# Kernel optimization log

Hardware: AMD Instinct MI355X
Metric: run time of the kernel (lower is better)

Reference implementation:

```python
import jax, jax.numpy as jnp
import numpy as np

B, L, D, H, FF, V, NL = 1024, 200, 128, 4, 512, 100001, 2
DK = D // H
EPS = 1e-5


def layer_norm(x, w, b):
    mu = jnp.mean(x, axis=-1, keepdims=True)
    var = jnp.mean(jnp.square(x - mu), axis=-1, keepdims=True)
    return (x - mu) * jax.lax.rsqrt(var + EPS) * w + b


def setup_inputs() -> dict:
    key = jax.random.key(0)
    ks = jax.random.split(key, 32)
    s = 0.02
    d = {}
    d["batch_seqs"] = jax.random.randint(ks[0], (B, L), 0, V, dtype=jnp.int32)
    d["token_emb"] = jax.random.normal(ks[1], (V, D), jnp.float32) * s
    d["pos_emb"] = jax.random.normal(ks[2], (L, D), jnp.float32) * s
    # per-layer stacked params, leading axis = layer
    d["Wq"] = jax.random.normal(ks[3], (NL, D, D), jnp.float32) * s
    d["bq"] = jnp.zeros((NL, D), jnp.float32)
    d["Wk"] = jax.random.normal(ks[4], (NL, D, D), jnp.float32) * s
    d["bk"] = jnp.zeros((NL, D), jnp.float32)
    d["Wv"] = jax.random.normal(ks[5], (NL, D, D), jnp.float32) * s
    d["bv"] = jnp.zeros((NL, D), jnp.float32)
    d["Wo"] = jax.random.normal(ks[6], (NL, D, D), jnp.float32) * s
    d["bo"] = jnp.zeros((NL, D), jnp.float32)
    d["ln1_w"] = jnp.ones((NL, D), jnp.float32)
    d["ln1_b"] = jnp.zeros((NL, D), jnp.float32)
    d["ln2_w"] = jnp.ones((NL, D), jnp.float32)
    d["ln2_b"] = jnp.zeros((NL, D), jnp.float32)
    d["W1"] = jax.random.normal(ks[7], (NL, D, FF), jnp.float32) * s
    d["b1"] = jnp.zeros((NL, FF), jnp.float32)
    d["W2"] = jax.random.normal(ks[8], (NL, FF, D), jnp.float32) * s
    d["b2"] = jnp.zeros((NL, D), jnp.float32)
    d["fc_W"] = jax.random.normal(ks[9], (L * D, D), jnp.float32) * s
    d["fc_b"] = jnp.zeros((D,), jnp.float32)
    return d


def reference(batch_seqs, token_emb, pos_emb, Wq, bq, Wk, bk, Wv, bv, Wo, bo,
              ln1_w, ln1_b, ln2_w, ln2_b, W1, b1, W2, b2, fc_W, fc_b):
    # key-padding mask: [B,1,1,L] (broadcasts over heads and queries)
    mask = (batch_seqs > 0)[:, None, None, :]
    x = token_emb[batch_seqs] + pos_emb[None, :, :]  # [B,L,D]
    scale = 1.0 / jnp.sqrt(jnp.float32(DK))
    for i in range(NL):
        h = layer_norm(x, ln1_w[i], ln1_b[i])
        q = (h @ Wq[i] + bq[i]).reshape(B, L, H, DK)
        k = (h @ Wk[i] + bk[i]).reshape(B, L, H, DK)
        v = (h @ Wv[i] + bv[i]).reshape(B, L, H, DK)
        scores = jnp.einsum('bqhd,bkhd->bhqk', q, k) * scale
        scores = jnp.where(mask, scores, -1e9)
        p = jax.nn.softmax(scores, axis=-1)
        attn = jnp.einsum('bhqk,bkhd->bqhd', p, v).reshape(B, L, D)
        x = x + (attn @ Wo[i] + bo[i])
        h = layer_norm(x, ln2_w[i], ln2_b[i])
        ffn = jax.nn.gelu(h @ W1[i] + b1[i], approximate=False) @ W2[i] + b2[i]
        x = x + ffn
    # FlattenLayers: flatten [B, L*D] -> Linear -> [B, D]
    out = x.reshape(B, L * D) @ fc_W + fc_b
    return out
```

## Files before the change

### kernel.cpp

```cpp
#include <hip/hip_runtime.h>
#include <math.h>

typedef unsigned short u16;
typedef unsigned int u32;
typedef __attribute__((ext_vector_type(8))) short bf16x8;
typedef __attribute__((ext_vector_type(4))) float f32x4;

#define Bx 1024
#define Lx 200
#define Dx 128
#define FFx 512
#define Mx (Bx*Lx)
#define PVP 232
#define TSP 40

__device__ __forceinline__ u16 f2bf(float f) {
  u32 u = __float_as_uint(f);
  u32 r = (u + 0x7fffu + ((u >> 16) & 1u)) >> 16;
  return (u16)r;
}

__device__ __forceinline__ float gelu_f(float v) {
  float z = v * fmaf(v * v, 0.0713548163f, 1.5957691216f);
  float e = __expf(-z);
  return v * __builtin_amdgcn_rcpf(1.0f + e);
}

union BFCV { u32 u[4]; bf16x8 h; };

__global__ void k_cvt(const float* __restrict__ src, u16* __restrict__ dst,
                      int N, int k_steps) {
  int id = blockIdx.x * 256 + threadIdx.x;
  int lane = id & 63;
  int rest = id >> 6;
  int kst = rest % k_steps;
  int ntile = rest / k_steps;
  int n = ntile * 16 + (lane & 15);
  int kb = kst * 32 + ((lane >> 4) << 3);
  const float* sp = src + (size_t)kb * N + n;
  u32 w[4];
  #pragma unroll
  for (int j = 0; j < 4; ++j) {
    u32 lo = f2bf(sp[(size_t)(2 * j) * N]);
    u32 hi = f2bf(sp[(size_t)(2 * j + 1) * N]);
    w[j] = lo | (hi << 16);
  }
  ((uint4*)dst)[id] = make_uint4(w[0], w[1], w[2], w[3]);
}

__global__ void k_embed(const int* __restrict__ seq, const float* __restrict__ tok,
                        const float* __restrict__ pos, float* __restrict__ x) {
  const int i = blockIdx.x * 256 + threadIdx.x;
  const int row = i >> 5, c = i & 31;
  const int t = seq[row];
  const int l = row % Lx;
  const float4 a = ((const float4*)tok)[(size_t)t * 32 + c];
  const float4 p = ((const float4*)pos)[l * 32 + c];
  ((float4*)x)[i] = make_float4(a.x + p.x, a.y + p.y, a.z + p.z, a.w + p.w);
}

__device__ __forceinline__ void reg_ln(const float* __restrict__ xr,
                                       const float* __restrict__ ln_w,
                                       const float* __restrict__ ln_b,
                                       int quad, bf16x8 af[4]) {
  float v[32];
  float s = 0.f, sq = 0.f;
  #pragma unroll
  for (int kst = 0; kst < 4; ++kst) {
    float4 a = *(const float4*)(xr + kst * 32);
    float4 b = *(const float4*)(xr + kst * 32 + 4);
    v[kst * 8 + 0] = a.x; v[kst * 8 + 1] = a.y; v[kst * 8 + 2] = a.z; v[kst * 8 + 3] = a.w;
    v[kst * 8 + 4] = b.x; v[kst * 8 + 5] = b.y; v[kst * 8 + 6] = b.z; v[kst * 8 + 7] = b.w;
  }
  #pragma unroll
  for (int i = 0; i < 32; ++i) { s += v[i]; sq = fmaf(v[i], v[i], sq); }
  s  += __shfl_xor(s, 16);  s  += __shfl_xor(s, 32);
  sq += __shfl_xor(sq, 16); sq += __shfl_xor(sq, 32);
  float mu = s * 0.0078125f;
  float rr = rsqrtf(fmaf(-mu, mu, sq * 0.0078125f) + 1e-5f);
  #pragma unroll
  for (int kst = 0; kst < 4; ++kst) {
    const float* lwp = ln_w + kst * 32 + quad * 8;
    const float* lbp = ln_b + kst * 32 + quad * 8;
    float4 lw0 = *(const float4*)(lwp);
    float4 lw1 = *(const float4*)(lwp + 4);
    float4 lb0 = *(const float4*)(lbp);
    float4 lb1 = *(const float4*)(lbp + 4);
    float hw[8] = {lw0.x, lw0.y, lw0.z, lw0.w, lw1.x, lw1.y, lw1.z, lw1.w};
    float hb[8] = {lb0.x, lb0.y, lb0.z, lb0.w, lb1.x, lb1.y, lb1.z, lb1.w};
    BFCV cv;
    #pragma unroll
    for (int j = 0; j < 4; ++j) {
      float h0 = fmaf((v[kst * 8 + 2 * j]     - mu) * rr, hw[2 * j],     hb[2 * j]);
      float h1 = fmaf((v[kst * 8 + 2 * j + 1] - mu) * rr, hw[2 * j + 1], hb[2 * j + 1]);
      cv.u[j] = (u32)f2bf(h0) | ((u32)f2bf(h1) << 16);
    }
    af[kst] = cv.h;
  }
}

__global__ __launch_bounds__(256, 4)
void k_qkv(const float* __restrict__ x, const float* __restrict__ ln_w,
           const float* __restrict__ ln_b, const u16* __restrict__ Wqkvs,
           const float* __restrict__ bq, const float* __restrict__ bk,
           const float* __restrict__ bv,
           u16* __restrict__ qo, u16* __restrict__ ko, u16* __restrict__ vo) {
  const int tid = threadIdx.x;
  const int row0 = blockIdx.x * 64;
  const int lane = tid & 63, wv = tid >> 6;
  const int l15 = lane & 15, quad = lane >> 4;
  const int m0 = wv * 16;

  bf16x8 af[4];
  reg_ln(x + (size_t)(row0 + m0 + l15) * Dx + quad * 8, ln_w, ln_b, quad, af);

  int bl[4], ll[4];
  #pragma unroll
  for (int r = 0; r < 4; ++r) {
    int gr = row0 + m0 + quad * 4 + r;
    bl[r] = gr / 200;
    ll[r] = gr - bl[r] * 200;
  }

  const float scale = 0.17677669529663687f;
  #pragma unroll
  for (int nt = 0; nt < 24; ++nt) {
    f32x4 acc = (f32x4){0.f, 0.f, 0.f, 0.f};
    const u16* wb = Wqkvs + ((size_t)(nt * 4) * 64 + lane) * 8;
    #pragma unroll
    for (int kst = 0; kst < 4; ++kst) {
      bf16x8 bfr = *(const bf16x8*)(wb + kst * 64 * 8);
      acc = __builtin_amdgcn_mfma_f32_16x16x32_bf16(af[kst], bfr, acc, 0, 0, 0);
    }
    const int col = (nt & 7) * 16 + l15;
    const int head = col >> 5, dk = col & 31;
    if (nt < 8) {
      float bb = bq[col];
      #pragma unroll
      for (int r = 0; r < 4; ++r)
        qo[((size_t)(bl[r] * 4 + head) * 200 + ll[r]) * 32 + dk] = f2bf((acc[r] + bb) * scale);
    } else if (nt < 16) {
      float bb = bk[col];
      #pragma unroll
      for (int r = 0; r < 4; ++r)
        ko[((size_t)(bl[r] * 4 + head) * 200 + ll[r]) * 32 + dk] = f2bf(acc[r] + bb);
    } else {
      float bb = bv[col];
      #pragma unroll
      for (int r = 0; r < 4; ++r)
        vo[((size_t)(bl[r] * 4 + head) * 200 + ll[r]) * 32 + dk] = f2bf(acc[r] + bb);
    }
  }
}

__global__ __launch_bounds__(256, 3)
void k_attn2(const u16* __restrict__ q, const u16* __restrict__ k,
             const u16* __restrict__ v, const int* __restrict__ seq,
             u16* __restrict__ attn) {
  __shared__ float smask[224];
  __shared__ __align__(16) u16 vt[32 * PVP];
  __shared__ __align__(16) u16 Pb[4][16 * PVP];
  const int tid = threadIdx.x;
  const int bl = blockIdx.x >> 2, head = blockIdx.x & 3;
  const int bh = blockIdx.x;
  const int lane = tid & 63, wv = tid >> 6;
  const int l15 = lane & 15, quad = lane >> 4;

  if (tid < 224)
    smask[tid] = (tid < 200 && seq[bl * 200 + tid] > 0) ? 0.f : -1e9f;
  #pragma unroll 1
  for (int e = tid; e < 800; e += 256) {
    int l = e >> 2, g = (e & 3) * 8;
    uint4 pv = *(const uint4*)(v + ((size_t)bh * 200 + l) * 32 + g);
    const u16* pw = (const u16*)&pv;
    #pragma unroll
    for (int j = 0; j < 8; ++j) vt[(g + j) * PVP + l] = pw[j];
  }
  #pragma unroll 1
  for (int e = tid; e < 1024; e += 256) {
    int rr = e >> 5, cc = 200 + (e & 31);
    vt[rr * PVP + cc] = 0;
  }
  __syncthreads();

  float msk[14];
  #pragma unroll
  for (int nt = 0; nt < 14; ++nt) msk[nt] = smask[nt * 16 + l15];

  const u16* qbase = q + (size_t)bh * 200 * 32;
  const u16* kbase = k + (size_t)bh * 200 * 32;
  u16* Pw = Pb[wv];

  #pragma unroll 1
  for (int mt = wv; mt < 13; mt += 4) {
    bf16x8 qf = *(const bf16x8*)(qbase + (mt * 16 + l15) * 32 + quad * 8);
    f32x4 s[14];
    #pragma unroll
    for (int nt = 0; nt < 14; ++nt) {
      bf16x8 kf = *(const bf16x8*)(kbase + (nt * 16 + l15) * 32 + quad * 8);
      s[nt] = __builtin_amdgcn_mfma_f32_16x16x32_bf16(qf, kf, (f32x4){0.f, 0.f, 0.f, 0.f}, 0, 0, 0);
    }
    float rmax[4] = {-1e30f, -1e30f, -1e30f, -1e30f};
    #pragma unroll
    for (int nt = 0; nt < 14; ++nt) {
      #pragma unroll
      for (int r = 0; r < 4; ++r) {
        s[nt][r] += msk[nt];
        rmax[r] = fmaxf(rmax[r], s[nt][r]);
      }
    }
    #pragma unroll
    for (int m = 1; m < 16; m <<= 1) {
      #pragma unroll
      for (int r = 0; r < 4; ++r) rmax[r] = fmaxf(rmax[r], __shfl_xor(rmax[r], m));
    }
    float rsum[4] = {0.f, 0.f, 0.f, 0.f};
    #pragma unroll
    for (int nt = 0; nt < 14; ++nt) {
      #pragma unroll
      for (int r = 0; r < 4; ++r) {
        float p = __expf(s[nt][r] - rmax[r]);
        s[nt][r] = p;
        rsum[r] += p;
      }
    }
    #pragma unroll
    for (int m = 1; m < 16; m <<= 1) {
      #pragma unroll
      for (int r = 0; r < 4; ++r) rsum[r] += __shfl_xor(rsum[r], m);
    }
    float inv[4];
    #pragma unroll
    for (int r = 0; r < 4; ++r) inv[r] = 1.0f / rsum[r];
    #pragma unroll
    for (int nt = 0; nt < 14; ++nt) {
      #pragma unroll
      for (int r = 0; r < 4; ++r)
        Pw[(quad * 4 + r) * PVP + nt * 16 + l15] = f2bf(s[nt][r]);
    }
    __asm__ __volatile__("s_waitcnt lgkmcnt(0)" ::: "memory");
    f32x4 o0 = (f32x4){0.f, 0.f, 0.f, 0.f}, o1 = (f32x4){0.f, 0.f, 0.f, 0.f};
    #pragma unroll
    for (int kst = 0; kst < 7; ++kst) {
      bf16x8 pf  = *(const bf16x8*)&Pw[l15 * PVP + kst * 32 + quad * 8];
      bf16x8 vf0 = *(const bf16x8*)&vt[l15 * PVP + kst * 32 + quad * 8];
      bf16x8 vf1 = *(const bf16x8*)&vt[(16 + l15) * PVP + kst * 32 + quad * 8];
      o0 = __builtin_amdgcn_mfma_f32_16x16x32_bf16(pf, vf0, o0, 0, 0, 0);
      o1 = __builtin_amdgcn_mfma_f32_16x16x32_bf16(pf, vf1, o1, 0, 0, 0);
    }
    #pragma unroll
    for (int r = 0; r < 4; ++r) {
      int row = mt * 16 + quad * 4 + r;
      if (row < 200) {
        u16* op = attn + ((size_t)bl * 200 + row) * 128 + head * 32;
        op[l15]      = f2bf(o0[r] * inv[r]);
        op[16 + l15] = f2bf(o1[r] * inv[r]);
      }
    }
  }
}

__global__ __launch_bounds__(256, 4)
void k_oproj(const u16* __restrict__ a, const u16* __restrict__ Wos,
             const float* __restrict__ bo, float* __restrict__ x) {
  const int tid = threadIdx.x;
  const int lane = tid & 63, wv = tid >> 6;
  const int l15 = lane & 15, quad = lane >> 4;
  const size_t m0 = (size_t)blockIdx.x * 64 + wv * 16;
  f32x4 acc[8];
  #pragma unroll
  for (int i = 0; i < 8; ++i) acc[i] = (f32x4){0.f, 0.f, 0.f, 0.f};
  #pragma unroll
  for (int kst = 0; kst < 4; ++kst) {
    bf16x8 af = *(const bf16x8*)(a + (m0 + l15) * Dx + kst * 32 + quad * 8);
    const u16* wb = Wos + (kst * 64 + lane) * 8;
    #pragma unroll
    for (int nt = 0; nt < 8; ++nt) {
      bf16x8 bf = *(const bf16x8*)(wb + nt * (4 * 64 * 8));
      acc[nt] = __builtin_amdgcn_mfma_f32_16x16x32_bf16(af, bf, acc[nt], 0, 0, 0);
    }
  }
  #pragma unroll
  for (int nt = 0; nt < 8; ++nt) {
    int col = nt * 16 + l15;
    float bb = bo[col];
    #pragma unroll
    for (int r = 0; r < 4; ++r) {
      size_t idx = (m0 + quad * 4 + r) * Dx + col;
      x[idx] += acc[nt][r] + bb;
    }
  }
}

__global__ __launch_bounds__(512, 4)
void k_ffn(float* __restrict__ x, const float* __restrict__ ln_w,
           const float* __restrict__ ln_b,
           const u16* __restrict__ W1s, const float* __restrict__ b1,
           const u16* __restrict__ W2s, const float* __restrict__ b2) {
  __shared__ __align__(16) u16 smem[5120 + 8192 + 8192];
  u16* ts  = smem;
  u16* w1b = smem + 5120;
  u16* w2b = smem + 13312;
  const int tid = threadIdx.x;
  const size_t row0 = (size_t)blockIdx.x * 128;
  const int lane = tid & 63, wv = tid >> 6;
  const int l15 = lane & 15, quad = lane >> 4;
  const int m0 = wv * 16;
  const int snt = wv, soff = lane;

  bf16x8 af[4];
  reg_ln(x + (row0 + m0 + l15) * (size_t)Dx + quad * 8, ln_w, ln_b, quad, af);

  ((uint4*)w1b)[tid] = ((const uint4*)(W1s + (size_t)(snt * 4) * 512))[soff];
  ((uint4*)w2b)[tid] = ((const uint4*)(W2s + (size_t)(snt * 16) * 512))[soff];
  __syncthreads();

  f32x4 acc2[8];
  #pragma unroll
  for (int i = 0; i < 8; ++i) acc2[i] = (f32x4){0.f, 0.f, 0.f, 0.f};

  #pragma unroll 1
  for (int ch = 0; ch < 4; ++ch) {
    f32x4 acc1[8];
    #pragma unroll
    for (int i = 0; i < 8; ++i) acc1[i] = (f32x4){0.f, 0.f, 0.f, 0.f};
    #pragma unroll
    for (int kst = 0; kst < 4; ++kst) {
      uint4 stg;
      if (kst < 3)
        stg = ((const uint4*)(W1s + (size_t)((ch * 8 + snt) * 4 + kst + 1) * 512))[soff];
      const u16* wb = w1b + (kst & 1) * 4096;
      #pragma unroll
      for (int nt = 0; nt < 8; ++nt) {
        bf16x8 bfr = *(const bf16x8*)&wb[nt * 512 + lane * 8];
        acc1[nt] = __builtin_amdgcn_mfma_f32_16x16x32_bf16(af[kst], bfr, acc1[nt], 0, 0, 0);
      }
      if (kst < 3)
        ((uint4*)(w1b + ((kst + 1) & 1) * 4096))[tid] = stg;
      __syncthreads();
    }
    #pragma unroll
    for (int p = 0; p < 4; ++p) {
      uint4 stg2, stg1;
      const bool s2  = (p < 3);
      const bool s1n = (p == 3) && (ch < 3);
      if (s2)
        stg2 = ((const uint4*)(W2s + (size_t)(snt * 16 + ch * 4 + p + 1) * 512))[soff];
      if (s1n) {
        stg1 = ((const uint4*)(W1s + (size_t)((ch + 1) * 8 + snt) * 4 * 512))[soff];
        stg2 = ((const uint4*)(W2s + (size_t)(snt * 16 + (ch + 1) * 4) * 512))[soff];
      }
      #pragma unroll
      for (int q2 = 0; q2 < 2; ++q2) {
        const int ntg = 2 * p + q2;
        float bb = b1[ch * 128 + ntg * 16 + l15];
        #pragma unroll
        for (int r = 0; r < 4; ++r)
          ts[(m0 + quad * 4 + r) * TSP + q2 * 16 + l15] =
              f2bf(gelu_f(acc1[ntg][r] + bb));
      }
      __asm__ __volatile__("s_waitcnt lgkmcnt(0)" ::: "memory");
      bf16x8 tf = *(const bf16x8*)&ts[(m0 + l15) * TSP + quad * 8];
      const u16* wb = w2b + (p & 1) * 4096;
      #pragma unroll
      for (int nt = 0; nt < 8; ++nt) {
        bf16x8 bfr = *(const bf16x8*)&wb[nt * 512 + lane * 8];
        acc2[nt] = __builtin_amdgcn_mfma_f32_16x16x32_bf16(tf, bfr, acc2[nt], 0, 0, 0);
      }
      if (s2)
        ((uint4*)(w2b + ((p + 1) & 1) * 4096))[tid] = stg2;
      if (s1n) {
        ((uint4*)w1b)[tid] = stg1;
        ((uint4*)w2b)[tid] = stg2;
      }
      __syncthreads();
    }
  }
  #pragma unroll
  for (int nt = 0; nt < 8; ++nt) {
    int col = nt * 16 + l15;
    float bb = b2[col];
    #pragma unroll
    for (int r = 0; r < 4; ++r) {
      size_t idx = (row0 + m0 + quad * 4 + r) * Dx + col;
      x[idx] += acc2[nt][r] + bb;
    }
  }
}

__global__ __launch_bounds__(256, 4)
void k_fc(const float* __restrict__ x, const u16* __restrict__ fcWs,
          float* __restrict__ part) {
  const int tid = threadIdx.x;
  const int lane = tid & 63, wv = tid >> 6;
  const int l15 = lane & 15, quad = lane >> 4;
  const int m0 = blockIdx.x * 64 + wv * 16;
  const int ky = blockIdx.y;
  f32x4 acc[8];
  #pragma unroll
  for (int i = 0; i < 8; ++i) acc[i] = (f32x4){0.f, 0.f, 0.f, 0.f};
  const float* xp = x + (size_t)(m0 + l15) * 25600 + quad * 8;
  #pragma unroll 1
  for (int kst = ky * 25; kst < ky * 25 + 25; ++kst) {
    float4 xa = *(const float4*)(xp + kst * 32);
    float4 xb2 = *(const float4*)(xp + kst * 32 + 4);
    bf16x8 af;
    af[0] = (short)f2bf(xa.x);  af[1] = (short)f2bf(xa.y);
    af[2] = (short)f2bf(xa.z);  af[3] = (short)f2bf(xa.w);
    af[4] = (short)f2bf(xb2.x); af[5] = (short)f2bf(xb2.y);
    af[6] = (short)f2bf(xb2.z); af[7] = (short)f2bf(xb2.w);
    const u16* wb = fcWs + ((size_t)kst * 64 + lane) * 8;
    #pragma unroll
    for (int nt = 0; nt < 8; ++nt) {
      bf16x8 bf = *(const bf16x8*)(wb + (size_t)nt * (800 * 64 * 8));
      acc[nt] = __builtin_amdgcn_mfma_f32_16x16x32_bf16(af, bf, acc[nt], 0, 0, 0);
    }
  }
  float* pp = part + (size_t)ky * (Bx * Dx);
  #pragma unroll
  for (int nt = 0; nt < 8; ++nt) {
    #pragma unroll
    for (int r = 0; r < 4; ++r) {
      pp[(size_t)(m0 + quad * 4 + r) * Dx + nt * 16 + l15] = acc[nt][r];
    }
  }
}

__global__ void k_fcred(const float* __restrict__ part, const float* __restrict__ fcb,
                        float* __restrict__ out) {
  int i = blockIdx.x * 256 + threadIdx.x;
  float s = fcb[i & 127];
  #pragma unroll
  for (int k = 0; k < 32; ++k) s += part[(size_t)k * (Bx * Dx) + i];
  out[i] = s;
}

extern "C" void kernel_launch(void* const* d_in, const int* in_sizes, int n_in,
                              void* d_out, int out_size, void* d_ws, size_t ws_size,
                              hipStream_t stream) {
  const int*   seq  = (const int*)d_in[0];
  const float* tok  = (const float*)d_in[1];
  const float* pos  = (const float*)d_in[2];
  const float* Wq   = (const float*)d_in[3];
  const float* bq   = (const float*)d_in[4];
  const float* Wk   = (const float*)d_in[5];
  const float* bk   = (const float*)d_in[6];
  const float* Wv   = (const float*)d_in[7];
  const float* bv   = (const float*)d_in[8];
  const float* Wo   = (const float*)d_in[9];
  const float* bo   = (const float*)d_in[10];
  const float* ln1w = (const float*)d_in[11];
  const float* ln1b = (const float*)d_in[12];
  const float* ln2w = (const float*)d_in[13];
  const float* ln2b = (const float*)d_in[14];
  const float* W1   = (const float*)d_in[15];
  const float* b1   = (const float*)d_in[16];
  const float* W2   = (const float*)d_in[17];
  const float* b2   = (const float*)d_in[18];
  const float* fcW  = (const float*)d_in[19];
  const float* fcb  = (const float*)d_in[20];
  float* out = (float*)d_out;

  char* ws = (char*)d_ws;
  const size_t XB = (size_t)Mx * Dx * 4;
  const size_t WBSZ = 7340032;

  int nc = 4;
  for (int t = 1; t <= 4; t <<= 1) {
    size_t qsz = (size_t)(Bx / t) * 51200;
    if (XB + 4 * qsz + WBSZ <= ws_size) { nc = t; break; }
  }
  const int BC = Bx / nc;
  const size_t qsz = (size_t)BC * 51200;

  float* x    = (float*)ws;
  u16* qb     = (u16*)(ws + XB);
  u16* kb     = (u16*)(ws + XB + qsz);
  u16* vb     = (u16*)(ws + XB + 2 * qsz);
  u16* ab     = (u16*)(ws + XB + 3 * qsz);
  float* part = (float*)(ws + XB);
  char* WB    = ws + XB + 4 * qsz;
  u16* W1s0   = (u16*)(WB);
  u16* W1s1   = (u16*)(WB + 131072);
  u16* W2s0   = (u16*)(WB + 262144);
  u16* W2s1   = (u16*)(WB + 393216);
  u16* Wos0   = (u16*)(WB + 524288);
  u16* Wos1   = (u16*)(WB + 557056);
  u16* Wqkvs0 = (u16*)(WB + 589824);
  u16* Wqkvs1 = (u16*)(WB + 688128);
  u16* fcWs   = (u16*)(WB + 786432);

  k_cvt<<<32, 256, 0, stream>>>(W1, W1s0, FFx, 4);
  k_cvt<<<32, 256, 0, stream>>>(W1 + Dx * FFx, W1s1, FFx, 4);
  k_cvt<<<32, 256, 0, stream>>>(W2, W2s0, Dx, 16);
  k_cvt<<<32, 256, 0, stream>>>(W2 + FFx * Dx, W2s1, Dx, 16);
  k_cvt<<<8, 256, 0, stream>>>(Wo, Wos0, Dx, 4);
  k_cvt<<<8, 256, 0, stream>>>(Wo + Dx * Dx, Wos1, Dx, 4);
  k_cvt<<<8, 256, 0, stream>>>(Wq, Wqkvs0, Dx, 4);
  k_cvt<<<8, 256, 0, stream>>>(Wk, Wqkvs0 + 16384, Dx, 4);
  k_cvt<<<8, 256, 0, stream>>>(Wv, Wqkvs0 + 32768, Dx, 4);
  k_cvt<<<8, 256, 0, stream>>>(Wq + Dx * Dx, Wqkvs1, Dx, 4);
  k_cvt<<<8, 256, 0, stream>>>(Wk + Dx * Dx, Wqkvs1 + 16384, Dx, 4);
  k_cvt<<<8, 256, 0, stream>>>(Wv + Dx * Dx, Wqkvs1 + 32768, Dx, 4);
  k_cvt<<<1600, 256, 0, stream>>>(fcW, fcWs, Dx, 800);

  k_embed<<<25600, 256, 0, stream>>>(seq, tok, pos, x);
  const int cblk = BC * 200 / 64;
  for (int i = 0; i < 2; ++i) {
    const u16* Wqkvs = (i == 0) ? Wqkvs0 : Wqkvs1;
    const u16* Wos   = (i == 0) ? Wos0 : Wos1;
    for (int c = 0; c < nc; ++c) {
      const float* xc = x + (size_t)c * BC * 200 * 128;
      k_qkv<<<cblk, 256, 0, stream>>>(xc, ln1w + i * Dx, ln1b + i * Dx, Wqkvs,
                                      bq + i * Dx, bk + i * Dx, bv + i * Dx,
                                      qb, kb, vb);
      k_attn2<<<BC * 4, 256, 0, stream>>>(qb, kb, vb, seq + (size_t)c * BC * 200, ab);
      k_oproj<<<cblk, 256, 0, stream>>>(ab, Wos, bo + i * Dx, (float*)xc);
    }
    k_ffn<<<1600, 512, 0, stream>>>(x, ln2w + i * Dx, ln2b + i * Dx,
                                    (i == 0) ? W1s0 : W1s1, b1 + i * FFx,
                                    (i == 0) ? W2s0 : W2s1, b2 + i * Dx);
  }
  k_fc<<<dim3(16, 32), 256, 0, stream>>>(x, fcWs, part);
  k_fcred<<<512, 256, 0, stream>>>(part, fcb, out);
}
```

Before: 976.6 us.

## Fuse embedding into first QKV kernel and retile FFN warps for weight reuse

Removes the standalone embedding kernel. The first layer's QKV kernel now gathers token and position embeddings, writes x, and applies layer norm in registers, which saves one full read and write pass of x. The FFN kernel is retiled so each of 8 warps computes a 32-row by 64-column tile. Each weight fragment loaded from LDS now feeds two MFMAs, and a single shared double-buffered weight stream replaces the separate W1 and W2 buffers. The GELU intermediate is stored as a full 128-column padded tile, which raises LDS use per block and could lower occupancy.

```diff
diff --git a/kernel.cpp b/kernel.cpp
--- a/kernel.cpp
+++ b/kernel.cpp
@@ -12,7 +12,7 @@
 #define FFx 512
 #define Mx (Bx*Lx)
 #define PVP 232
-#define TSP 40
+#define LNP 136
 
 __device__ __forceinline__ u16 f2bf(float f) {
   u32 u = __float_as_uint(f);
@@ -48,30 +48,11 @@
   ((uint4*)dst)[id] = make_uint4(w[0], w[1], w[2], w[3]);
 }
 
-__global__ void k_embed(const int* __restrict__ seq, const float* __restrict__ tok,
-                        const float* __restrict__ pos, float* __restrict__ x) {
-  const int i = blockIdx.x * 256 + threadIdx.x;
-  const int row = i >> 5, c = i & 31;
-  const int t = seq[row];
-  const int l = row % Lx;
-  const float4 a = ((const float4*)tok)[(size_t)t * 32 + c];
-  const float4 p = ((const float4*)pos)[l * 32 + c];
-  ((float4*)x)[i] = make_float4(a.x + p.x, a.y + p.y, a.z + p.z, a.w + p.w);
-}
-
-__device__ __forceinline__ void reg_ln(const float* __restrict__ xr,
-                                       const float* __restrict__ ln_w,
-                                       const float* __restrict__ ln_b,
-                                       int quad, bf16x8 af[4]) {
-  float v[32];
+__device__ __forceinline__ void ln_pack(const float v[32],
+                                        const float* __restrict__ ln_w,
+                                        const float* __restrict__ ln_b,
+                                        int quad, bf16x8 af[4]) {
   float s = 0.f, sq = 0.f;
-  #pragma unroll
-  for (int kst = 0; kst < 4; ++kst) {
-    float4 a = *(const float4*)(xr + kst * 32);
-    float4 b = *(const float4*)(xr + kst * 32 + 4);
-    v[kst * 8 + 0] = a.x; v[kst * 8 + 1] = a.y; v[kst * 8 + 2] = a.z; v[kst * 8 + 3] = a.w;
-    v[kst * 8 + 4] = b.x; v[kst * 8 + 5] = b.y; v[kst * 8 + 6] = b.z; v[kst * 8 + 7] = b.w;
-  }
   #pragma unroll
   for (int i = 0; i < 32; ++i) { s += v[i]; sq = fmaf(v[i], v[i], sq); }
   s  += __shfl_xor(s, 16);  s  += __shfl_xor(s, 32);
@@ -99,58 +80,118 @@
   }
 }
 
+__device__ __forceinline__ void load_x32(const float* __restrict__ xr, float v[32]) {
+  #pragma unroll
+  for (int kst = 0; kst < 4; ++kst) {
+    float4 a = *(const float4*)(xr + kst * 32);
+    float4 b = *(const float4*)(xr + kst * 32 + 4);
+    v[kst * 8 + 0] = a.x; v[kst * 8 + 1] = a.y; v[kst * 8 + 2] = a.z; v[kst * 8 + 3] = a.w;
+    v[kst * 8 + 4] = b.x; v[kst * 8 + 5] = b.y; v[kst * 8 + 6] = b.z; v[kst * 8 + 7] = b.w;
+  }
+}
+
+template <bool EMB>
+__device__ __forceinline__ void qkv_body(
+    const float* __restrict__ x, float* __restrict__ xw,
+    const int* __restrict__ seqc, const float* __restrict__ tok,
+    const float* __restrict__ pos,
+    const float* __restrict__ ln_w, const float* __restrict__ ln_b,
+    const u16* __restrict__ Wqkvs,
+    const float* __restrict__ bq, const float* __restrict__ bk,
+    const float* __restrict__ bv,
+    u16* __restrict__ qo, u16* __restrict__ ko, u16* __restrict__ vo) {
+  const int tid = threadIdx.x;
+  const int row0 = blockIdx.x * 64;
+  const int lane = tid & 63, wv = tid >> 6;
+  const int l15 = lane & 15, quad = lane >> 4;
+  const int m0 = wv * 16;
+  const int gr_ln = row0 + m0 + l15;
+
+  float v[32];
+  if (EMB) {
+    const int t = seqc[gr_ln];
+    const int pl = gr_ln % 200;
+    const float* tp = tok + (size_t)t * Dx + quad * 8;
+    const float* pp = pos + (size_t)pl * Dx + quad * 8;
+    float* xp = xw + (size_t)gr_ln * Dx + quad * 8;
+    #pragma unroll
+    for (int kst = 0; kst < 4; ++kst) {
+      float4 a = *(const float4*)(tp + kst * 32);
+      float4 b = *(const float4*)(tp + kst * 32 + 4);
+      float4 p0 = *(const float4*)(pp + kst * 32);
+      float4 p1 = *(const float4*)(pp + kst * 32 + 4);
+      a.x += p0.x; a.y += p0.y; a.z += p0.z; a.w += p0.w;
+      b.x += p1.x; b.y += p1.y; b.z += p1.z; b.w += p1.w;
+      *(float4*)(xp + kst * 32)     = a;
+      *(float4*)(xp + kst * 32 + 4) = b;
+      v[kst * 8 + 0] = a.x; v[kst * 8 + 1] = a.y; v[kst * 8 + 2] = a.z; v[kst * 8 + 3] = a.w;
+      v[kst * 8 + 4] = b.x; v[kst * 8 + 5] = b.y; v[kst * 8 + 6] = b.z; v[kst * 8 + 7] = b.w;
+    }
+  } else {
+    load_x32(x + (size_t)gr_ln * Dx + quad * 8, v);
+  }
+  bf16x8 af[4];
+  ln_pack(v, ln_w, ln_b, quad, af);
+
+  int bl[4], ll[4];
+  #pragma unroll
+  for (int r = 0; r < 4; ++r) {
+    int gr = row0 + m0 + quad * 4 + r;
+    bl[r] = gr / 200;
+    ll[r] = gr - bl[r] * 200;
+  }
+
+  const float scale = 0.17677669529663687f;
+  #pragma unroll
+  for (int nt = 0; nt < 24; ++nt) {
+    f32x4 acc = (f32x4){0.f, 0.f, 0.f, 0.f};
+    const u16* wb = Wqkvs + ((size_t)(nt * 4) * 64 + lane) * 8;
+    #pragma unroll
+    for (int kst = 0; kst < 4; ++kst) {
+      bf16x8 bfr = *(const bf16x8*)(wb + kst * 64 * 8);
+      acc = __builtin_amdgcn_mfma_f32_16x16x32_bf16(af[kst], bfr, acc, 0, 0, 0);
+    }
+    const int col = (nt & 7) * 16 + l15;
+    const int head = col >> 5, dk = col & 31;
+    if (nt < 8) {
+      float bb = bq[col];
+      #pragma unroll
+      for (int r = 0; r < 4; ++r)
+        qo[((size_t)(bl[r] * 4 + head) * 200 + ll[r]) * 32 + dk] = f2bf((acc[r] + bb) * scale);
+    } else if (nt < 16) {
+      float bb = bk[col];
+      #pragma unroll
+      for (int r = 0; r < 4; ++r)
+        ko[((size_t)(bl[r] * 4 + head) * 200 + ll[r]) * 32 + dk] = f2bf(acc[r] + bb);
+    } else {
+      float bb = bv[col];
+      #pragma unroll
+      for (int r = 0; r < 4; ++r)
+        vo[((size_t)(bl[r] * 4 + head) * 200 + ll[r]) * 32 + dk] = f2bf(acc[r] + bb);
+    }
+  }
+}
+
 __global__ __launch_bounds__(256, 4)
 void k_qkv(const float* __restrict__ x, const float* __restrict__ ln_w,
            const float* __restrict__ ln_b, const u16* __restrict__ Wqkvs,
            const float* __restrict__ bq, const float* __restrict__ bk,
            const float* __restrict__ bv,
            u16* __restrict__ qo, u16* __restrict__ ko, u16* __restrict__ vo) {
-  const int tid = threadIdx.x;
-  const int row0 = blockIdx.x * 64;
-  const int lane = tid & 63, wv = tid >> 6;
-  const int l15 = lane & 15, quad = lane >> 4;
-  const int m0 = wv * 16;
-
-  bf16x8 af[4];
-  reg_ln(x + (size_t)(row0 + m0 + l15) * Dx + quad * 8, ln_w, ln_b, quad, af);
-
-  int bl[4], ll[4];
-  #pragma unroll
-  for (int r = 0; r < 4; ++r) {
-    int gr = row0 + m0 + quad * 4 + r;
-    bl[r] = gr / 200;
-    ll[r] = gr - bl[r] * 200;
-  }
-
-  const float scale = 0.17677669529663687f;
-  #pragma unroll
-  for (int nt = 0; nt < 24; ++nt) {
-    f32x4 acc = (f32x4){0.f, 0.f, 0.f, 0.f};
-    const u16* wb = Wqkvs + ((size_t)(nt * 4) * 64 + lane) * 8;
-    #pragma unroll
-    for (int kst = 0; kst < 4; ++kst) {
-      bf16x8 bfr = *(const bf16x8*)(wb + kst * 64 * 8);
-      acc = __builtin_amdgcn_mfma_f32_16x16x32_bf16(af[kst], bfr, acc, 0, 0, 0);
-    }
-    const int col = (nt & 7) * 16 + l15;
-    const int head = col >> 5, dk = col & 31;
-    if (nt < 8) {
-      float bb = bq[col];
-      #pragma unroll
-      for (int r = 0; r < 4; ++r)
-        qo[((size_t)(bl[r] * 4 + head) * 200 + ll[r]) * 32 + dk] = f2bf((acc[r] + bb) * scale);
-    } else if (nt < 16) {
-      float bb = bk[col];
-      #pragma unroll
-      for (int r = 0; r < 4; ++r)
-        ko[((size_t)(bl[r] * 4 + head) * 200 + ll[r]) * 32 + dk] = f2bf(acc[r] + bb);
-    } else {
-      float bb = bv[col];
-      #pragma unroll
-      for (int r = 0; r < 4; ++r)
-        vo[((size_t)(bl[r] * 4 + head) * 200 + ll[r]) * 32 + dk] = f2bf(acc[r] + bb);
-    }
-  }
+  qkv_body<false>(x, nullptr, nullptr, nullptr, nullptr, ln_w, ln_b, Wqkvs,
+                  bq, bk, bv, qo, ko, vo);
+}
+
+__global__ __launch_bounds__(256, 4)
+void k_qkv_emb(float* __restrict__ xw, const int* __restrict__ seqc,
+               const float* __restrict__ tok, const float* __restrict__ pos,
+               const float* __restrict__ ln_w, const float* __restrict__ ln_b,
+               const u16* __restrict__ Wqkvs,
+               const float* __restrict__ bq, const float* __restrict__ bk,
+               const float* __restrict__ bv,
+               u16* __restrict__ qo, u16* __restrict__ ko, u16* __restrict__ vo) {
+  qkv_body<true>(nullptr, xw, seqc, tok, pos, ln_w, ln_b, Wqkvs,
+                 bq, bk, bv, qo, ko, vo);
 }
 
 __global__ __launch_bounds__(256, 3)
@@ -297,95 +338,116 @@
            const float* __restrict__ ln_b,
            const u16* __restrict__ W1s, const float* __restrict__ b1,
            const u16* __restrict__ W2s, const float* __restrict__ b2) {
-  __shared__ __align__(16) u16 smem[5120 + 8192 + 8192];
-  u16* ts  = smem;
-  u16* w1b = smem + 5120;
-  u16* w2b = smem + 13312;
+  __shared__ __align__(16) u16 ts[128 * LNP];
+  __shared__ __align__(16) u16 wbuf[2 * 4096];
   const int tid = threadIdx.x;
   const size_t row0 = (size_t)blockIdx.x * 128;
   const int lane = tid & 63, wv = tid >> 6;
   const int l15 = lane & 15, quad = lane >> 4;
-  const int m0 = wv * 16;
-  const int snt = wv, soff = lane;
-
-  bf16x8 af[4];
-  reg_ln(x + (row0 + m0 + l15) * (size_t)Dx + quad * 8, ln_w, ln_b, quad, af);
-
-  ((uint4*)w1b)[tid] = ((const uint4*)(W1s + (size_t)(snt * 4) * 512))[soff];
-  ((uint4*)w2b)[tid] = ((const uint4*)(W2s + (size_t)(snt * 16) * 512))[soff];
+  const int rg = wv >> 1, cq = wv & 1;
+  const int r0 = rg * 32;
+
+  bf16x8 af[2][4];
+  #pragma unroll
+  for (int rt = 0; rt < 2; ++rt) {
+    float v[32];
+    load_x32(x + (row0 + r0 + rt * 16 + l15) * (size_t)Dx + quad * 8, v);
+    ln_pack(v, ln_w, ln_b, quad, af[rt]);
+  }
+
+  ((uint4*)wbuf)[tid] = ((const uint4*)(W1s + (size_t)(wv * 4) * 512))[lane];
   __syncthreads();
 
-  f32x4 acc2[8];
-  #pragma unroll
-  for (int i = 0; i < 8; ++i) acc2[i] = (f32x4){0.f, 0.f, 0.f, 0.f};
-
+  f32x4 acc2[2][4];
+  #pragma unroll
+  for (int rt = 0; rt < 2; ++rt)
+    #pragma unroll
+    for (int j = 0; j < 4; ++j) acc2[rt][j] = (f32x4){0.f, 0.f, 0.f, 0.f};
+
+  int pq = 0;
   #pragma unroll 1
   for (int ch = 0; ch < 4; ++ch) {
-    f32x4 acc1[8];
-    #pragma unroll
-    for (int i = 0; i < 8; ++i) acc1[i] = (f32x4){0.f, 0.f, 0.f, 0.f};
+    f32x4 acc1[2][4];
+    #pragma unroll
+    for (int rt = 0; rt < 2; ++rt)
+      #pragma unroll
+      for (int j = 0; j < 4; ++j) acc1[rt][j] = (f32x4){0.f, 0.f, 0.f, 0.f};
     #pragma unroll
     for (int kst = 0; kst < 4; ++kst) {
       uint4 stg;
       if (kst < 3)
-        stg = ((const uint4*)(W1s + (size_t)((ch * 8 + snt) * 4 + kst + 1) * 512))[soff];
-      const u16* wb = w1b + (kst & 1) * 4096;
-      #pragma unroll
-      for (int nt = 0; nt < 8; ++nt) {
-        bf16x8 bfr = *(const bf16x8*)&wb[nt * 512 + lane * 8];
-        acc1[nt] = __builtin_amdgcn_mfma_f32_16x16x32_bf16(af[kst], bfr, acc1[nt], 0, 0, 0);
-      }
-      if (kst < 3)
-        ((uint4*)(w1b + ((kst + 1) & 1) * 4096))[tid] = stg;
+        stg = ((const uint4*)(W1s + (size_t)((ch * 8 + wv) * 4 + kst + 1) * 512))[lane];
+      else
+        stg = ((const uint4*)(W2s + (size_t)(wv * 16 + ch * 4) * 512))[lane];
+      const u16* wb = wbuf + (pq & 1) * 4096;
+      bf16x8 bfr[4];
+      #pragma unroll
+      for (int j = 0; j < 4; ++j)
+        bfr[j] = *(const bf16x8*)&wb[(cq * 4 + j) * 512 + lane * 8];
+      #pragma unroll
+      for (int j = 0; j < 4; ++j) {
+        acc1[0][j] = __builtin_amdgcn_mfma_f32_16x16x32_bf16(af[0][kst], bfr[j], acc1[0][j], 0, 0, 0);
+        acc1[1][j] = __builtin_amdgcn_mfma_f32_16x16x32_bf16(af[1][kst], bfr[j], acc1[1][j], 0, 0, 0);
+      }
+      if (kst == 3) {
+        #pragma unroll
+        for (int rt = 0; rt < 2; ++rt)
+          #pragma unroll
+          for (int j = 0; j < 4; ++j) {
+            const int col = (cq * 4 + j) * 16 + l15;
+            float bb = b1[ch * 128 + col];
+            #pragma unroll
+            for (int r = 0; r < 4; ++r)
+              ts[(r0 + rt * 16 + quad * 4 + r) * LNP + col] =
+                  f2bf(gelu_f(acc1[rt][j][r] + bb));
+          }
+      }
+      ((uint4*)(wbuf + ((pq + 1) & 1) * 4096))[tid] = stg;
       __syncthreads();
+      ++pq;
     }
     #pragma unroll
     for (int p = 0; p < 4; ++p) {
-      uint4 stg2, stg1;
-      const bool s2  = (p < 3);
-      const bool s1n = (p == 3) && (ch < 3);
-      if (s2)
-        stg2 = ((const uint4*)(W2s + (size_t)(snt * 16 + ch * 4 + p + 1) * 512))[soff];
-      if (s1n) {
-        stg1 = ((const uint4*)(W1s + (size_t)((ch + 1) * 8 + snt) * 4 * 512))[soff];
-        stg2 = ((const uint4*)(W2s + (size_t)(snt * 16 + (ch + 1) * 4) * 512))[soff];
-      }
-      #pragma unroll
-      for (int q2 = 0; q2 < 2; ++q2) {
-        const int ntg = 2 * p + q2;
-        float bb = b1[ch * 128 + ntg * 16 + l15];
-        #pragma unroll
-        for (int r = 0; r < 4; ++r)
-          ts[(m0 + quad * 4 + r) * TSP + q2 * 16 + l15] =
-              f2bf(gelu_f(acc1[ntg][r] + bb));
-      }
-      __asm__ __volatile__("s_waitcnt lgkmcnt(0)" ::: "memory");
-      bf16x8 tf = *(const bf16x8*)&ts[(m0 + l15) * TSP + quad * 8];
-      const u16* wb = w2b + (p & 1) * 4096;
-      #pragma unroll
-      for (int nt = 0; nt < 8; ++nt) {
-        bf16x8 bfr = *(const bf16x8*)&wb[nt * 512 + lane * 8];
-        acc2[nt] = __builtin_amdgcn_mfma_f32_16x16x32_bf16(tf, bfr, acc2[nt], 0, 0, 0);
-      }
-      if (s2)
-        ((uint4*)(w2b + ((p + 1) & 1) * 4096))[tid] = stg2;
-      if (s1n) {
-        ((uint4*)w1b)[tid] = stg1;
-        ((uint4*)w2b)[tid] = stg2;
-      }
+      uint4 stg;
+      bool have = true;
+      if (p < 3)
+        stg = ((const uint4*)(W2s + (size_t)(wv * 16 + ch * 4 + p + 1) * 512))[lane];
+      else if (ch < 3)
+        stg = ((const uint4*)(W1s + (size_t)(((ch + 1) * 8 + wv) * 4) * 512))[lane];
+      else
+        have = false;
+      const u16* wb = wbuf + (pq & 1) * 4096;
+      bf16x8 tf[2];
+      #pragma unroll
+      for (int rt = 0; rt < 2; ++rt)
+        tf[rt] = *(const bf16x8*)&ts[(r0 + rt * 16 + l15) * LNP + p * 32 + quad * 8];
+      bf16x8 bfr[4];
+      #pragma unroll
+      for (int j = 0; j < 4; ++j)
+        bfr[j] = *(const bf16x8*)&wb[(cq * 4 + j) * 512 + lane * 8];
+      #pragma unroll
+      for (int j = 0; j < 4; ++j) {
+        acc2[0][j] = __builtin_amdgcn_mfma_f32_16x16x32_bf16(tf[0], bfr[j], acc2[0][j], 0, 0, 0);
+        acc2[1][j] = __builtin_amdgcn_mfma_f32_16x16x32_bf16(tf[1], bfr[j], acc2[1][j], 0, 0, 0);
+      }
+      if (have)
+        ((uint4*)(wbuf + ((pq + 1) & 1) * 4096))[tid] = stg;
       __syncthreads();
-    }
-  }
-  #pragma unroll
-  for (int nt = 0; nt < 8; ++nt) {
-    int col = nt * 16 + l15;
-    float bb = b2[col];
-    #pragma unroll
-    for (int r = 0; r < 4; ++r) {
-      size_t idx = (row0 + m0 + quad * 4 + r) * Dx + col;
-      x[idx] += acc2[nt][r] + bb;
-    }
-  }
+      ++pq;
+    }
+  }
+  #pragma unroll
+  for (int rt = 0; rt < 2; ++rt)
+    #pragma unroll
+    for (int j = 0; j < 4; ++j) {
+      const int col = (cq * 4 + j) * 16 + l15;
+      float bb = b2[col];
+      #pragma unroll
+      for (int r = 0; r < 4; ++r) {
+        size_t idx = (row0 + r0 + rt * 16 + quad * 4 + r) * Dx + col;
+        x[idx] += acc2[rt][j][r] + bb;
+      }
+    }
 }
 
 __global__ __launch_bounds__(256, 4)
@@ -504,18 +566,23 @@
   k_cvt<<<8, 256, 0, stream>>>(Wv + Dx * Dx, Wqkvs1 + 32768, Dx, 4);
   k_cvt<<<1600, 256, 0, stream>>>(fcW, fcWs, Dx, 800);
 
-  k_embed<<<25600, 256, 0, stream>>>(seq, tok, pos, x);
   const int cblk = BC * 200 / 64;
   for (int i = 0; i < 2; ++i) {
     const u16* Wqkvs = (i == 0) ? Wqkvs0 : Wqkvs1;
     const u16* Wos   = (i == 0) ? Wos0 : Wos1;
     for (int c = 0; c < nc; ++c) {
-      const float* xc = x + (size_t)c * BC * 200 * 128;
-      k_qkv<<<cblk, 256, 0, stream>>>(xc, ln1w + i * Dx, ln1b + i * Dx, Wqkvs,
-                                      bq + i * Dx, bk + i * Dx, bv + i * Dx,
-                                      qb, kb, vb);
-      k_attn2<<<BC * 4, 256, 0, stream>>>(qb, kb, vb, seq + (size_t)c * BC * 200, ab);
-      k_oproj<<<cblk, 256, 0, stream>>>(ab, Wos, bo + i * Dx, (float*)xc);
+      float* xc = x + (size_t)c * BC * 200 * 128;
+      const int* seqc = seq + (size_t)c * BC * 200;
+      if (i == 0)
+        k_qkv_emb<<<cblk, 256, 0, stream>>>(xc, seqc, tok, pos,
+                                            ln1w, ln1b, Wqkvs,
+                                            bq, bk, bv, qb, kb, vb);
+      else
+        k_qkv<<<cblk, 256, 0, stream>>>(xc, ln1w + i * Dx, ln1b + i * Dx, Wqkvs,
+                                        bq + i * Dx, bk + i * Dx, bv + i * Dx,
+                                        qb, kb, vb);
+      k_attn2<<<BC * 4, 256, 0, stream>>>(qb, kb, vb, seqc, ab);
+      k_oproj<<<cblk, 256, 0, stream>>>(ab, Wos, bo + i * Dx, xc);
     }
     k_ffn<<<1600, 512, 0, stream>>>(x, ln2w + i * Dx, ln2b + i * Dx,
                                     (i == 0) ? W1s0 : W1s1, b1 + i * FFx,
```

After: 1.036 ms. 1.06x slower.

## Split attention query tiles across two blocks and batch weight conversions

Applied to the files above, without the earlier changes.

Each (batch, head) attention block is split into two blocks that handle query tiles 0-6 and 7-12, doubling grid size so waves are better balanced: in the old scheme the first wave took four of the thirteen query tiles. Each half block still loads the full V transpose and mask, so that staging work is duplicated. The thirteen separate weight-conversion launches are merged into one launch with a job table, which removes launch overhead.

```diff
diff --git a/kernel.cpp b/kernel.cpp
--- a/kernel.cpp
+++ b/kernel.cpp
@@ -28,9 +28,23 @@
 
 union BFCV { u32 u[4]; bf16x8 h; };
 
-__global__ void k_cvt(const float* __restrict__ src, u16* __restrict__ dst,
-                      int N, int k_steps) {
-  int id = blockIdx.x * 256 + threadIdx.x;
+struct CvtJobs {
+  const float* src[13];
+  u16* dst[13];
+  int N[13];
+  int ks[13];
+  int bstart[14];
+};
+
+__global__ void k_cvt_all(CvtJobs J) {
+  const int b = blockIdx.x;
+  int j = 0;
+  #pragma unroll 1
+  while (b >= J.bstart[j + 1]) ++j;
+  const float* __restrict__ src = J.src[j];
+  u16* __restrict__ dst = J.dst[j];
+  const int N = J.N[j], k_steps = J.ks[j];
+  int id = (b - J.bstart[j]) * 256 + threadIdx.x;
   int lane = id & 63;
   int rest = id >> 6;
   int kst = rest % k_steps;
@@ -40,10 +54,10 @@
   const float* sp = src + (size_t)kb * N + n;
   u32 w[4];
   #pragma unroll
-  for (int j = 0; j < 4; ++j) {
-    u32 lo = f2bf(sp[(size_t)(2 * j) * N]);
-    u32 hi = f2bf(sp[(size_t)(2 * j + 1) * N]);
-    w[j] = lo | (hi << 16);
+  for (int jj = 0; jj < 4; ++jj) {
+    u32 lo = f2bf(sp[(size_t)(2 * jj) * N]);
+    u32 hi = f2bf(sp[(size_t)(2 * jj + 1) * N]);
+    w[jj] = lo | (hi << 16);
   }
   ((uint4*)dst)[id] = make_uint4(w[0], w[1], w[2], w[3]);
 }
@@ -161,8 +175,9 @@
   __shared__ __align__(16) u16 vt[32 * PVP];
   __shared__ __align__(16) u16 Pb[4][16 * PVP];
   const int tid = threadIdx.x;
-  const int bl = blockIdx.x >> 2, head = blockIdx.x & 3;
-  const int bh = blockIdx.x;
+  const int bl = blockIdx.x >> 3, head = (blockIdx.x >> 1) & 3;
+  const int bh = blockIdx.x >> 1;
+  const int half = blockIdx.x & 1;
   const int lane = tid & 63, wv = tid >> 6;
   const int l15 = lane & 15, quad = lane >> 4;
 
@@ -191,8 +206,10 @@
   const u16* kbase = k + (size_t)bh * 200 * 32;
   u16* Pw = Pb[wv];
 
+  const int mt0 = half ? 7 : 0;
+  const int mte = half ? 13 : 7;
   #pragma unroll 1
-  for (int mt = wv; mt < 13; mt += 4) {
+  for (int mt = mt0 + wv; mt < mte; mt += 4) {
     bf16x8 qf = *(const bf16x8*)(qbase + (mt * 16 + l15) * 32 + quad * 8);
     f32x4 s[14];
     #pragma unroll
@@ -490,19 +507,26 @@
   u16* Wqkvs1 = (u16*)(WB + 688128);
   u16* fcWs   = (u16*)(WB + 786432);
 
-  k_cvt<<<32, 256, 0, stream>>>(W1, W1s0, FFx, 4);
-  k_cvt<<<32, 256, 0, stream>>>(W1 + Dx * FFx, W1s1, FFx, 4);
-  k_cvt<<<32, 256, 0, stream>>>(W2, W2s0, Dx, 16);
-  k_cvt<<<32, 256, 0, stream>>>(W2 + FFx * Dx, W2s1, Dx, 16);
-  k_cvt<<<8, 256, 0, stream>>>(Wo, Wos0, Dx, 4);
-  k_cvt<<<8, 256, 0, stream>>>(Wo + Dx * Dx, Wos1, Dx, 4);
-  k_cvt<<<8, 256, 0, stream>>>(Wq, Wqkvs0, Dx, 4);
-  k_cvt<<<8, 256, 0, stream>>>(Wk, Wqkvs0 + 16384, Dx, 4);
-  k_cvt<<<8, 256, 0, stream>>>(Wv, Wqkvs0 + 32768, Dx, 4);
-  k_cvt<<<8, 256, 0, stream>>>(Wq + Dx * Dx, Wqkvs1, Dx, 4);
-  k_cvt<<<8, 256, 0, stream>>>(Wk + Dx * Dx, Wqkvs1 + 16384, Dx, 4);
-  k_cvt<<<8, 256, 0, stream>>>(Wv + Dx * Dx, Wqkvs1 + 32768, Dx, 4);
-  k_cvt<<<1600, 256, 0, stream>>>(fcW, fcWs, Dx, 800);
+  CvtJobs J;
+  const float* srcs[13] = {W1, W1 + Dx * FFx, W2, W2 + FFx * Dx,
+                           Wo, Wo + Dx * Dx,
+                           Wq, Wk, Wv,
+                           Wq + Dx * Dx, Wk + Dx * Dx, Wv + Dx * Dx,
+                           fcW};
+  u16* dsts[13] = {W1s0, W1s1, W2s0, W2s1, Wos0, Wos1,
+                   Wqkvs0, Wqkvs0 + 16384, Wqkvs0 + 32768,
+                   Wqkvs1, Wqkvs1 + 16384, Wqkvs1 + 32768,
+                   fcWs};
+  const int Ns[13]  = {FFx, FFx, Dx, Dx, Dx, Dx, Dx, Dx, Dx, Dx, Dx, Dx, Dx};
+  const int kss[13] = {4, 4, 16, 16, 4, 4, 4, 4, 4, 4, 4, 4, 800};
+  const int nblk[13] = {32, 32, 32, 32, 8, 8, 8, 8, 8, 8, 8, 8, 1600};
+  int acc = 0;
+  for (int j = 0; j < 13; ++j) {
+    J.src[j] = srcs[j]; J.dst[j] = dsts[j]; J.N[j] = Ns[j]; J.ks[j] = kss[j];
+    J.bstart[j] = acc; acc += nblk[j];
+  }
+  J.bstart[13] = acc;
+  k_cvt_all<<<acc, 256, 0, stream>>>(J);
 
   k_embed<<<25600, 256, 0, stream>>>(seq, tok, pos, x);
   const int cblk = BC * 200 / 64;
@@ -510,12 +534,13 @@
     const u16* Wqkvs = (i == 0) ? Wqkvs0 : Wqkvs1;
     const u16* Wos   = (i == 0) ? Wos0 : Wos1;
     for (int c = 0; c < nc; ++c) {
-      const float* xc = x + (size_t)c * BC * 200 * 128;
+      float* xc = x + (size_t)c * BC * 200 * 128;
+      const int* seqc = seq + (size_t)c * BC * 200;
       k_qkv<<<cblk, 256, 0, stream>>>(xc, ln1w + i * Dx, ln1b + i * Dx, Wqkvs,
                                       bq + i * Dx, bk + i * Dx, bv + i * Dx,
                                       qb, kb, vb);
-      k_attn2<<<BC * 4, 256, 0, stream>>>(qb, kb, vb, seq + (size_t)c * BC * 200, ab);
-      k_oproj<<<cblk, 256, 0, stream>>>(ab, Wos, bo + i * Dx, (float*)xc);
+      k_attn2<<<BC * 8, 256, 0, stream>>>(qb, kb, vb, seqc, ab);
+      k_oproj<<<cblk, 256, 0, stream>>>(ab, Wos, bo + i * Dx, xc);
     }
     k_ffn<<<1600, 512, 0, stream>>>(x, ln2w + i * Dx, ln2b + i * Dx,
                                     (i == 0) ? W1s0 : W1s1, b1 + i * FFx,
```

Measured after the change: 988.9 us. No clear change (+1.3%).
